# Performance work log

Hardware: AMD Instinct MI355X
Metric: run time of the kernel (lower is better)

The kernel has to match this reference:

```python
import jax, jax.numpy as jnp
import numpy as np

B = 16384
MOTION = 128      # motion_size
USED = 3          # used_motions
LAT = 32          # latent_size
H1 = 512
H2 = 512
MOE = 8
IN = MOTION * (USED - 1) + LAT  # 288 (used_angles = 0)


def setup_inputs() -> dict:
    key = jax.random.key(0)
    ks = jax.random.split(key, 14)
    s = 0.02
    return {
        "motions": jax.random.normal(ks[0], (B, MOTION * (USED - 1)), jnp.float32),
        "z": jax.random.normal(ks[1], (B, LAT), jnp.float32),
        # gate MLP params
        "gw1": jax.random.normal(ks[2], (IN, H1), jnp.float32) * s,
        "gb1": jnp.zeros((H1,), jnp.float32),
        "gw2": jax.random.normal(ks[3], (H1, H2), jnp.float32) * s,
        "gb2": jnp.zeros((H2,), jnp.float32),
        "gw3": jax.random.normal(ks[4], (H2, MOE), jnp.float32) * s,
        "gb3": jnp.zeros((MOE,), jnp.float32),
        # stacked expert params: layer k weight [MOE, in_k, out_k]
        "W1": jax.random.normal(ks[5], (MOE, IN, H1), jnp.float32) * s,
        "b1": jnp.zeros((MOE, H1), jnp.float32),
        "W2": jax.random.normal(ks[6], (MOE, H1 + LAT, H2), jnp.float32) * s,
        "b2": jnp.zeros((MOE, H2), jnp.float32),
        "W3": jax.random.normal(ks[7], (MOE, H2 + LAT, MOTION), jnp.float32) * s,
        "b3": jnp.zeros((MOE, MOTION), jnp.float32),
    }


def reference(motions, z, gw1, gb1, gw2, gb2, gw3, gb3, W1, b1, W2, b2, W3, b3):
    # used_angles == 0 -> angles is empty; input = concat([motions, z])
    x = jnp.concatenate([motions, z], axis=1)            # [B, IN]

    # gate: 3-layer ELU MLP -> per-expert blend weights [B, MOE]
    para = jax.nn.elu(x @ gw1 + gb1)
    para = jax.nn.elu(para @ gw2 + gb2)
    para = jax.nn.elu(para @ gw3 + gb3)

    # all experts batched via stacked weights (replaces Python loop)
    zb = jnp.broadcast_to(z[None], (MOE, B, LAT))        # z re-concatenated per layer
    h = jax.nn.elu(jnp.einsum('bi,eio->ebo', x, W1) + b1[:, None, :])              # [E,B,H1]
    h = jax.nn.elu(jnp.einsum('ebi,eio->ebo', jnp.concatenate([h, zb], -1), W2)
                   + b2[:, None, :])                                               # [E,B,H2]
    h = jax.nn.elu(jnp.einsum('ebi,eio->ebo', jnp.concatenate([h, zb], -1), W3)
                   + b3[:, None, :])                                               # [E,B,M]

    # gated combine, then divide by Frobenius norm of the whole gate matrix
    out = jnp.einsum('be,ebm->bm', para, h)              # [B, MOTION]
    out = out / jnp.linalg.norm(para)
    return jax.nn.sigmoid(out)
```

## Files before the change

### kernel.cpp

```cpp
#include <hip/hip_runtime.h>


typedef __attribute__((ext_vector_type(8))) short bf16x8;
typedef __attribute__((ext_vector_type(4))) float f32x4;
#define MFMA(a, b, c) __builtin_amdgcn_mfma_f32_16x16x32_bf16(a, b, c, 0, 0, 0)

#define STRIDE 552

__device__ __forceinline__ float elu_f(float x) { return x > 0.f ? x : (__expf(x) - 1.f); }

__device__ __forceinline__ ushort f2bf(float f) {
    union { float f; unsigned u; } v; v.f = f;
    unsigned r = v.u + 0x7fffu + ((v.u >> 16) & 1u);
    return (ushort)(r >> 16);
}
__device__ __forceinline__ float bf2f(ushort u) {
    union { unsigned u; float f; } v; v.u = ((unsigned)u) << 16;
    return v.f;
}

__global__ void prep_xz(const float* __restrict__ motions, const float* __restrict__ z,
                        ushort* __restrict__ xz) {
    int i = blockIdx.x * 256 + threadIdx.x;
    int r = i / 72, c = i % 72;
    float4 v = (c < 64) ? ((const float4*)motions)[r * 64 + c]
                        : ((const float4*)z)[r * 8 + (c - 64)];
    ushort4 o;
    o.x = f2bf(v.x); o.y = f2bf(v.y); o.z = f2bf(v.z); o.w = f2bf(v.w);
    *(ushort4*)(xz + (size_t)r * 288 + c * 4) = o;
}

__global__ void prep_transpose(const float* __restrict__ in, ushort* __restrict__ out,
                               int K, int N) {
    __shared__ float tile[32][33];
    const int e = blockIdx.z;
    const float* inp = in + (size_t)e * K * N;
    ushort* outp = out + (size_t)e * N * K;
    const int k0 = blockIdx.x * 32, n0 = blockIdx.y * 32;
    const int tx = threadIdx.x, ty = threadIdx.y;
    #pragma unroll
    for (int i = 0; i < 4; ++i)
        tile[ty + i * 8][tx] = inp[(size_t)(k0 + ty + i * 8) * N + n0 + tx];
    __syncthreads();
    #pragma unroll
    for (int i = 0; i < 4; ++i)
        outp[(size_t)(n0 + ty + i * 8) * K + k0 + tx] = f2bf(tile[tx][ty + i * 8]);
}

__global__ __launch_bounds__(512, 2) void gate_kernel(
    const ushort* __restrict__ xz,
    const ushort* __restrict__ gw1t, const float* __restrict__ gb1,
    const ushort* __restrict__ gw2t, const float* __restrict__ gb2,
    const float* __restrict__ gw3, const float* __restrict__ gb3,
    float* __restrict__ para, float* __restrict__ partial)
{
    __shared__ ushort hA[64 * STRIDE];
    __shared__ ushort hB[64 * STRIDE];
    __shared__ float red[512];
    const int t = threadIdx.x;
    const int lane = t & 63, w = t >> 6;
    const int lr = lane & 15, lk = lane >> 4;
    const int r0 = blockIdx.x * 64;

    for (int i = t; i < 64 * 36; i += 512) {
        int r = i / 36, c = i % 36;
        *(uint4*)&hB[r * STRIDE + c * 8] = *(const uint4*)(xz + (size_t)(r0 + r) * 288 + c * 8);
    }
    __syncthreads();

    {
        f32x4 acc[4][4] = {};
        const int n0 = w * 64;
        for (int ks = 0; ks < 9; ++ks) {
            bf16x8 a[4], b[4];
            #pragma unroll
            for (int mf = 0; mf < 4; ++mf)
                a[mf] = *(const bf16x8*)&hB[(mf * 16 + lr) * STRIDE + ks * 32 + lk * 8];
            #pragma unroll
            for (int nf = 0; nf < 4; ++nf)
                b[nf] = *(const bf16x8*)(gw1t + (size_t)(n0 + nf * 16 + lr) * 288 + ks * 32 + lk * 8);
            #pragma unroll
            for (int mf = 0; mf < 4; ++mf)
                #pragma unroll
                for (int nf = 0; nf < 4; ++nf)
                    acc[mf][nf] = MFMA(a[mf], b[nf], acc[mf][nf]);
        }
        #pragma unroll
        for (int nf = 0; nf < 4; ++nf) {
            int col = n0 + nf * 16 + lr;
            float bb = gb1[col];
            #pragma unroll
            for (int mf = 0; mf < 4; ++mf)
                #pragma unroll
                for (int j = 0; j < 4; ++j)
                    hA[(mf * 16 + lk * 4 + j) * STRIDE + col] = f2bf(elu_f(acc[mf][nf][j] + bb));
        }
    }
    __syncthreads();

    {
        f32x4 acc[4][4] = {};
        const int n0 = w * 64;
        for (int ks = 0; ks < 16; ++ks) {
            bf16x8 a[4], b[4];
            #pragma unroll
            for (int mf = 0; mf < 4; ++mf)
                a[mf] = *(const bf16x8*)&hA[(mf * 16 + lr) * STRIDE + ks * 32 + lk * 8];
            #pragma unroll
            for (int nf = 0; nf < 4; ++nf)
                b[nf] = *(const bf16x8*)(gw2t + (size_t)(n0 + nf * 16 + lr) * 512 + ks * 32 + lk * 8);
            #pragma unroll
            for (int mf = 0; mf < 4; ++mf)
                #pragma unroll
                for (int nf = 0; nf < 4; ++nf)
                    acc[mf][nf] = MFMA(a[mf], b[nf], acc[mf][nf]);
        }
        #pragma unroll
        for (int nf = 0; nf < 4; ++nf) {
            int col = n0 + nf * 16 + lr;
            float bb = gb2[col];
            #pragma unroll
            for (int mf = 0; mf < 4; ++mf)
                #pragma unroll
                for (int j = 0; j < 4; ++j)
                    hB[(mf * 16 + lk * 4 + j) * STRIDE + col] = f2bf(elu_f(acc[mf][nf][j] + bb));
        }
    }
    __syncthreads();

    {
        const int row = t >> 3, e = t & 7;
        float acc = 0.f;
        for (int k = 0; k < 512; k += 8) {
            uint4 hv = *(const uint4*)&hB[row * STRIDE + k];
            acc += bf2f((ushort)(hv.x)) * gw3[(k + 0) * 8 + e];
            acc += bf2f((ushort)(hv.x >> 16)) * gw3[(k + 1) * 8 + e];
            acc += bf2f((ushort)(hv.y)) * gw3[(k + 2) * 8 + e];
            acc += bf2f((ushort)(hv.y >> 16)) * gw3[(k + 3) * 8 + e];
            acc += bf2f((ushort)(hv.z)) * gw3[(k + 4) * 8 + e];
            acc += bf2f((ushort)(hv.z >> 16)) * gw3[(k + 5) * 8 + e];
            acc += bf2f((ushort)(hv.w)) * gw3[(k + 6) * 8 + e];
            acc += bf2f((ushort)(hv.w >> 16)) * gw3[(k + 7) * 8 + e];
        }
        float p = elu_f(acc + gb3[e]);
        para[(size_t)(r0 + row) * 8 + e] = p;
        red[t] = p * p;
    }
    __syncthreads();
    for (int s = 256; s >= 1; s >>= 1) {
        if (t < s) red[t] += red[t + s];
        __syncthreads();
    }
    if (t == 0) partial[blockIdx.x] = red[0];
}

__global__ void finalize_kernel(const float* __restrict__ partial, float* __restrict__ invn) {
    __shared__ float red[256];
    const int t = threadIdx.x;
    red[t] = partial[t];
    __syncthreads();
    for (int s = 128; s >= 1; s >>= 1) {
        if (t < s) red[t] += red[t + s];
        __syncthreads();
    }
    if (t == 0) invn[0] = 1.0f / sqrtf(red[0]);
}

__global__ __launch_bounds__(512, 2) void expert_kernel(
    const ushort* __restrict__ xz, const float* __restrict__ z,
    const ushort* __restrict__ W1t, const float* __restrict__ b1,
    const ushort* __restrict__ W2t, const float* __restrict__ b2,
    const ushort* __restrict__ W3t, const float* __restrict__ b3,
    const float* __restrict__ para, const float* __restrict__ invn,
    float* __restrict__ out)
{
    __shared__ ushort hA[64 * STRIDE];
    __shared__ ushort hB[64 * STRIDE];
    __shared__ float ps[64 * 8];
    const int t = threadIdx.x;
    const int lane = t & 63, w = t >> 6;
    const int lr = lane & 15, lk = lane >> 4;
    const int r0 = blockIdx.x * 64;

    for (int i = t; i < 2048; i += 512) {
        int r = i >> 5, c = i & 31;
        ushort v = f2bf(z[(size_t)(r0 + r) * 32 + c]);
        hA[r * STRIDE + 512 + c] = v;
        hB[r * STRIDE + 512 + c] = v;
    }
    ps[t] = para[(size_t)r0 * 8 + t];
    const float inv_norm = invn[0];

    float oacc[4][4];
    #pragma unroll
    for (int mf = 0; mf < 4; ++mf)
        #pragma unroll
        for (int j = 0; j < 4; ++j) oacc[mf][j] = 0.f;

    for (int e = 0; e < 8; ++e) {
        __syncthreads();
        for (int i = t; i < 64 * 36; i += 512) {
            int r = i / 36, c = i % 36;
            *(uint4*)&hB[r * STRIDE + c * 8] = *(const uint4*)(xz + (size_t)(r0 + r) * 288 + c * 8);
        }
        __syncthreads();

        {
            const ushort* Wt = W1t + (size_t)e * 512 * 288;
            f32x4 acc[4][4] = {};
            const int n0 = w * 64;
            for (int ks = 0; ks < 9; ++ks) {
                bf16x8 a[4], b[4];
                #pragma unroll
                for (int mf = 0; mf < 4; ++mf)
                    a[mf] = *(const bf16x8*)&hB[(mf * 16 + lr) * STRIDE + ks * 32 + lk * 8];
                #pragma unroll
                for (int nf = 0; nf < 4; ++nf)
                    b[nf] = *(const bf16x8*)(Wt + (size_t)(n0 + nf * 16 + lr) * 288 + ks * 32 + lk * 8);
                #pragma unroll
                for (int mf = 0; mf < 4; ++mf)
                    #pragma unroll
                    for (int nf = 0; nf < 4; ++nf)
                        acc[mf][nf] = MFMA(a[mf], b[nf], acc[mf][nf]);
            }
            #pragma unroll
            for (int nf = 0; nf < 4; ++nf) {
                int col = n0 + nf * 16 + lr;
                float bb = b1[e * 512 + col];
                #pragma unroll
                for (int mf = 0; mf < 4; ++mf)
                    #pragma unroll
                    for (int j = 0; j < 4; ++j)
                        hA[(mf * 16 + lk * 4 + j) * STRIDE + col] = f2bf(elu_f(acc[mf][nf][j] + bb));
            }
        }
        __syncthreads();

        {
            const ushort* Wt = W2t + (size_t)e * 512 * 544;
            f32x4 acc[4][4] = {};
            const int n0 = w * 64;
            for (int ks = 0; ks < 17; ++ks) {
                bf16x8 a[4], b[4];
                #pragma unroll
                for (int mf = 0; mf < 4; ++mf)
                    a[mf] = *(const bf16x8*)&hA[(mf * 16 + lr) * STRIDE + ks * 32 + lk * 8];
                #pragma unroll
                for (int nf = 0; nf < 4; ++nf)
                    b[nf] = *(const bf16x8*)(Wt + (size_t)(n0 + nf * 16 + lr) * 544 + ks * 32 + lk * 8);
                #pragma unroll
                for (int mf = 0; mf < 4; ++mf)
                    #pragma unroll
                    for (int nf = 0; nf < 4; ++nf)
                        acc[mf][nf] = MFMA(a[mf], b[nf], acc[mf][nf]);
            }
            #pragma unroll
            for (int nf = 0; nf < 4; ++nf) {
                int col = n0 + nf * 16 + lr;
                float bb = b2[e * 512 + col];
                #pragma unroll
                for (int mf = 0; mf < 4; ++mf)
                    #pragma unroll
                    for (int j = 0; j < 4; ++j)
                        hB[(mf * 16 + lk * 4 + j) * STRIDE + col] = f2bf(elu_f(acc[mf][nf][j] + bb));
            }
        }
        __syncthreads();

        {
            const ushort* Wt = W3t + (size_t)e * 128 * 544;
            f32x4 acc3[4] = {};
            const int n0 = w * 16;
            for (int ks = 0; ks < 17; ++ks) {
                bf16x8 b = *(const bf16x8*)(Wt + (size_t)(n0 + lr) * 544 + ks * 32 + lk * 8);
                #pragma unroll
                for (int mf = 0; mf < 4; ++mf) {
                    bf16x8 a = *(const bf16x8*)&hB[(mf * 16 + lr) * STRIDE + ks * 32 + lk * 8];
                    acc3[mf] = MFMA(a, b, acc3[mf]);
                }
            }
            float bb = b3[e * 128 + n0 + lr];
            #pragma unroll
            for (int mf = 0; mf < 4; ++mf)
                #pragma unroll
                for (int j = 0; j < 4; ++j) {
                    int row = mf * 16 + lk * 4 + j;
                    float h3 = elu_f(acc3[mf][j] + bb);
                    oacc[mf][j] += ps[row * 8 + e] * h3;
                }
        }
    }

    #pragma unroll
    for (int mf = 0; mf < 4; ++mf)
        #pragma unroll
        for (int j = 0; j < 4; ++j) {
            int row = mf * 16 + lk * 4 + j;
            float v = oacc[mf][j] * inv_norm;
            out[(size_t)(r0 + row) * 128 + w * 16 + lr] = 1.0f / (1.0f + __expf(-v));
        }
}

extern "C" void kernel_launch(void* const* d_in, const int* in_sizes, int n_in,
                              void* d_out, int out_size, void* d_ws, size_t ws_size,
                              hipStream_t stream) {
    const float* motions = (const float*)d_in[0];
    const float* z   = (const float*)d_in[1];
    const float* gw1 = (const float*)d_in[2];
    const float* gb1 = (const float*)d_in[3];
    const float* gw2 = (const float*)d_in[4];
    const float* gb2 = (const float*)d_in[5];
    const float* gw3 = (const float*)d_in[6];
    const float* gb3 = (const float*)d_in[7];
    const float* W1  = (const float*)d_in[8];
    const float* b1  = (const float*)d_in[9];
    const float* W2  = (const float*)d_in[10];
    const float* b2  = (const float*)d_in[11];
    const float* W3  = (const float*)d_in[12];
    const float* b3  = (const float*)d_in[13];
    float* out = (float*)d_out;

    char* W = (char*)d_ws;
    ushort* xz      = (ushort*)(W);
    ushort* gw1t    = (ushort*)(W + 9437184);
    ushort* gw2t    = (ushort*)(W + 9732096);
    ushort* W1t     = (ushort*)(W + 10256384);
    ushort* W2t     = (ushort*)(W + 12615680);
    ushort* W3t     = (ushort*)(W + 17072128);
    float*  para    = (float*) (W + 18186240);
    float*  partial = (float*) (W + 18710528);
    float*  invn    = (float*) (W + 18711552);

    prep_xz<<<dim3(4608), dim3(256), 0, stream>>>(motions, z, xz);
    prep_transpose<<<dim3(9, 16, 1), dim3(32, 8), 0, stream>>>(gw1, gw1t, 288, 512);
    prep_transpose<<<dim3(16, 16, 1), dim3(32, 8), 0, stream>>>(gw2, gw2t, 512, 512);
    prep_transpose<<<dim3(9, 16, 8), dim3(32, 8), 0, stream>>>(W1, W1t, 288, 512);
    prep_transpose<<<dim3(17, 16, 8), dim3(32, 8), 0, stream>>>(W2, W2t, 544, 512);
    prep_transpose<<<dim3(17, 4, 8), dim3(32, 8), 0, stream>>>(W3, W3t, 544, 128);

    gate_kernel<<<dim3(256), dim3(512), 0, stream>>>(xz, gw1t, gb1, gw2t, gb2, gw3, gb3,
                                                     para, partial);
    finalize_kernel<<<dim3(1), dim3(256), 0, stream>>>(partial, invn);
    expert_kernel<<<dim3(256), dim3(512), 0, stream>>>(xz, z, W1t, b1, W2t, b2, W3t, b3,
                                                       para, invn, out);
}
```

Baseline: 308.4 us.

## Use single shared buffer and read X directly from global to raise occupancy

```diff
diff --git a/kernel.cpp b/kernel.cpp
--- a/kernel.cpp
+++ b/kernel.cpp
@@ -47,35 +47,29 @@
         outp[(size_t)(n0 + ty + i * 8) * K + k0 + tx] = f2bf(tile[tx][ty + i * 8]);
 }
 
-__global__ __launch_bounds__(512, 2) void gate_kernel(
+__global__ __launch_bounds__(512, 4) void gate_kernel(
     const ushort* __restrict__ xz,
     const ushort* __restrict__ gw1t, const float* __restrict__ gb1,
     const ushort* __restrict__ gw2t, const float* __restrict__ gb2,
     const float* __restrict__ gw3, const float* __restrict__ gb3,
     float* __restrict__ para, float* __restrict__ partial)
 {
-    __shared__ ushort hA[64 * STRIDE];
-    __shared__ ushort hB[64 * STRIDE];
+    __shared__ ushort hs[64 * STRIDE];
     __shared__ float red[512];
     const int t = threadIdx.x;
     const int lane = t & 63, w = t >> 6;
     const int lr = lane & 15, lk = lane >> 4;
     const int r0 = blockIdx.x * 64;
-
-    for (int i = t; i < 64 * 36; i += 512) {
-        int r = i / 36, c = i % 36;
-        *(uint4*)&hB[r * STRIDE + c * 8] = *(const uint4*)(xz + (size_t)(r0 + r) * 288 + c * 8);
-    }
-    __syncthreads();
+    const ushort* xrow = xz + (size_t)r0 * 288;
+    const int n0 = w * 64;
 
     {
         f32x4 acc[4][4] = {};
-        const int n0 = w * 64;
         for (int ks = 0; ks < 9; ++ks) {
             bf16x8 a[4], b[4];
             #pragma unroll
             for (int mf = 0; mf < 4; ++mf)
-                a[mf] = *(const bf16x8*)&hB[(mf * 16 + lr) * STRIDE + ks * 32 + lk * 8];
+                a[mf] = *(const bf16x8*)(xrow + (size_t)(mf * 16 + lr) * 288 + ks * 32 + lk * 8);
             #pragma unroll
             for (int nf = 0; nf < 4; ++nf)
                 b[nf] = *(const bf16x8*)(gw1t + (size_t)(n0 + nf * 16 + lr) * 288 + ks * 32 + lk * 8);
@@ -93,19 +87,18 @@
             for (int mf = 0; mf < 4; ++mf)
                 #pragma unroll
                 for (int j = 0; j < 4; ++j)
-                    hA[(mf * 16 + lk * 4 + j) * STRIDE + col] = f2bf(elu_f(acc[mf][nf][j] + bb));
+                    hs[(mf * 16 + lk * 4 + j) * STRIDE + col] = f2bf(elu_f(acc[mf][nf][j] + bb));
         }
     }
     __syncthreads();
 
     {
         f32x4 acc[4][4] = {};
-        const int n0 = w * 64;
         for (int ks = 0; ks < 16; ++ks) {
             bf16x8 a[4], b[4];
             #pragma unroll
             for (int mf = 0; mf < 4; ++mf)
-                a[mf] = *(const bf16x8*)&hA[(mf * 16 + lr) * STRIDE + ks * 32 + lk * 8];
+                a[mf] = *(const bf16x8*)&hs[(mf * 16 + lr) * STRIDE + ks * 32 + lk * 8];
             #pragma unroll
             for (int nf = 0; nf < 4; ++nf)
                 b[nf] = *(const bf16x8*)(gw2t + (size_t)(n0 + nf * 16 + lr) * 512 + ks * 32 + lk * 8);
@@ -115,6 +108,7 @@
                 for (int nf = 0; nf < 4; ++nf)
                     acc[mf][nf] = MFMA(a[mf], b[nf], acc[mf][nf]);
         }
+        __syncthreads();
         #pragma unroll
         for (int nf = 0; nf < 4; ++nf) {
             int col = n0 + nf * 16 + lr;
@@ -123,7 +117,7 @@
             for (int mf = 0; mf < 4; ++mf)
                 #pragma unroll
                 for (int j = 0; j < 4; ++j)
-                    hB[(mf * 16 + lk * 4 + j) * STRIDE + col] = f2bf(elu_f(acc[mf][nf][j] + bb));
+                    hs[(mf * 16 + lk * 4 + j) * STRIDE + col] = f2bf(elu_f(acc[mf][nf][j] + bb));
         }
     }
     __syncthreads();
@@ -132,7 +126,7 @@
         const int row = t >> 3, e = t & 7;
         float acc = 0.f;
         for (int k = 0; k < 512; k += 8) {
-            uint4 hv = *(const uint4*)&hB[row * STRIDE + k];
+            uint4 hv = *(const uint4*)&hs[row * STRIDE + k];
             acc += bf2f((ushort)(hv.x)) * gw3[(k + 0) * 8 + e];
             acc += bf2f((ushort)(hv.x >> 16)) * gw3[(k + 1) * 8 + e];
             acc += bf2f((ushort)(hv.y)) * gw3[(k + 2) * 8 + e];
@@ -166,7 +160,7 @@
     if (t == 0) invn[0] = 1.0f / sqrtf(red[0]);
 }
 
-__global__ __launch_bounds__(512, 2) void expert_kernel(
+__global__ __launch_bounds__(512, 4) void expert_kernel(
     const ushort* __restrict__ xz, const float* __restrict__ z,
     const ushort* __restrict__ W1t, const float* __restrict__ b1,
     const ushort* __restrict__ W2t, const float* __restrict__ b2,
@@ -174,19 +168,18 @@
     const float* __restrict__ para, const float* __restrict__ invn,
     float* __restrict__ out)
 {
-    __shared__ ushort hA[64 * STRIDE];
-    __shared__ ushort hB[64 * STRIDE];
+    __shared__ ushort hs[64 * STRIDE];
     __shared__ float ps[64 * 8];
     const int t = threadIdx.x;
     const int lane = t & 63, w = t >> 6;
     const int lr = lane & 15, lk = lane >> 4;
     const int r0 = blockIdx.x * 64;
+    const ushort* xrow = xz + (size_t)r0 * 288;
+    const int n0 = w * 64;
 
     for (int i = t; i < 2048; i += 512) {
         int r = i >> 5, c = i & 31;
-        ushort v = f2bf(z[(size_t)(r0 + r) * 32 + c]);
-        hA[r * STRIDE + 512 + c] = v;
-        hB[r * STRIDE + 512 + c] = v;
+        hs[r * STRIDE + 512 + c] = f2bf(z[(size_t)(r0 + r) * 32 + c]);
     }
     ps[t] = para[(size_t)r0 * 8 + t];
     const float inv_norm = invn[0];
@@ -199,21 +192,15 @@
 
     for (int e = 0; e < 8; ++e) {
         __syncthreads();
-        for (int i = t; i < 64 * 36; i += 512) {
-            int r = i / 36, c = i % 36;
-            *(uint4*)&hB[r * STRIDE + c * 8] = *(const uint4*)(xz + (size_t)(r0 + r) * 288 + c * 8);
-        }
-        __syncthreads();
 
         {
             const ushort* Wt = W1t + (size_t)e * 512 * 288;
             f32x4 acc[4][4] = {};
-            const int n0 = w * 64;
             for (int ks = 0; ks < 9; ++ks) {
                 bf16x8 a[4], b[4];
                 #pragma unroll
                 for (int mf = 0; mf < 4; ++mf)
-                    a[mf] = *(const bf16x8*)&hB[(mf * 16 + lr) * STRIDE + ks * 32 + lk * 8];
+                    a[mf] = *(const bf16x8*)(xrow + (size_t)(mf * 16 + lr) * 288 + ks * 32 + lk * 8);
                 #pragma unroll
                 for (int nf = 0; nf < 4; ++nf)
                     b[nf] = *(const bf16x8*)(Wt + (size_t)(n0 + nf * 16 + lr) * 288 + ks * 32 + lk * 8);
@@ -231,7 +218,7 @@
                 for (int mf = 0; mf < 4; ++mf)
                     #pragma unroll
                     for (int j = 0; j < 4; ++j)
-                        hA[(mf * 16 + lk * 4 + j) * STRIDE + col] = f2bf(elu_f(acc[mf][nf][j] + bb));
+                        hs[(mf * 16 + lk * 4 + j) * STRIDE + col] = f2bf(elu_f(acc[mf][nf][j] + bb));
             }
         }
         __syncthreads();
@@ -239,12 +226,11 @@
         {
             const ushort* Wt = W2t + (size_t)e * 512 * 544;
             f32x4 acc[4][4] = {};
-            const int n0 = w * 64;
             for (int ks = 0; ks < 17; ++ks) {
                 bf16x8 a[4], b[4];
                 #pragma unroll
                 for (int mf = 0; mf < 4; ++mf)
-                    a[mf] = *(const bf16x8*)&hA[(mf * 16 + lr) * STRIDE + ks * 32 + lk * 8];
+                    a[mf] = *(const bf16x8*)&hs[(mf * 16 + lr) * STRIDE + ks * 32 + lk * 8];
                 #pragma unroll
                 for (int nf = 0; nf < 4; ++nf)
                     b[nf] = *(const bf16x8*)(Wt + (size_t)(n0 + nf * 16 + lr) * 544 + ks * 32 + lk * 8);
@@ -254,6 +240,7 @@
                     for (int nf = 0; nf < 4; ++nf)
                         acc[mf][nf] = MFMA(a[mf], b[nf], acc[mf][nf]);
             }
+            __syncthreads();
             #pragma unroll
             for (int nf = 0; nf < 4; ++nf) {
                 int col = n0 + nf * 16 + lr;
@@ -262,7 +249,7 @@
                 for (int mf = 0; mf < 4; ++mf)
                     #pragma unroll
                     for (int j = 0; j < 4; ++j)
-                        hB[(mf * 16 + lk * 4 + j) * STRIDE + col] = f2bf(elu_f(acc[mf][nf][j] + bb));
+                        hs[(mf * 16 + lk * 4 + j) * STRIDE + col] = f2bf(elu_f(acc[mf][nf][j] + bb));
             }
         }
         __syncthreads();
@@ -270,16 +257,16 @@
         {
             const ushort* Wt = W3t + (size_t)e * 128 * 544;
             f32x4 acc3[4] = {};
-            const int n0 = w * 16;
+            const int c0 = w * 16;
             for (int ks = 0; ks < 17; ++ks) {
-                bf16x8 b = *(const bf16x8*)(Wt + (size_t)(n0 + lr) * 544 + ks * 32 + lk * 8);
+                bf16x8 b = *(const bf16x8*)(Wt + (size_t)(c0 + lr) * 544 + ks * 32 + lk * 8);
                 #pragma unroll
                 for (int mf = 0; mf < 4; ++mf) {
-                    bf16x8 a = *(const bf16x8*)&hB[(mf * 16 + lr) * STRIDE + ks * 32 + lk * 8];
+                    bf16x8 a = *(const bf16x8*)&hs[(mf * 16 + lr) * STRIDE + ks * 32 + lk * 8];
                     acc3[mf] = MFMA(a, b, acc3[mf]);
                 }
             }
-            float bb = b3[e * 128 + n0 + lr];
+            float bb = b3[e * 128 + c0 + lr];
             #pragma unroll
             for (int mf = 0; mf < 4; ++mf)
                 #pragma unroll
```

After: 436.1 us. +41.4%, slower.
